# Performance work log

Measured on AMD Instinct MI355X. Metric: run time of the kernel, lower is better.

## Reference

```python
import jax, jax.numpy as jnp
import numpy as np

CHEB = jnp.array([676.5203681218851, -1259.1392167224028, 771.3234287776531,
                  -176.6150291621406, 12.507343278686905, -0.13857109526572012,
                  9.984369578019572e-06, 1.5056327351493116e-07], dtype=jnp.float32)
TWO_PI = float(np.sqrt(2.0 * np.pi))  # sqrt(2*pi), matches torch two_pi constant


def _gamma(z):
    # Lanczos approximation, 8 Chebyshev terms
    x = jnp.full_like(z, 0.9999999999998099)
    for i in range(8):
        x = x + CHEB[i] / (z + (i + 1.0))
    t = z + 8.0 - 0.5
    y = TWO_PI * t ** (z + 0.5) * jnp.exp(-t) * x
    return y / z


def _lower_incl_gamma(s, x, iters=8):
    it = iters - 2
    gs = _gamma(s)
    L = x ** s * gs * jnp.exp(-x)
    gs = gs * s
    R = jnp.reciprocal(gs) * jnp.ones_like(x)
    X = x
    for k in range(it):
        gs = gs * (s + k + 1)
        R = R + X / gs
        X = X * x
    gs = gs * (s + it + 1)
    R = R + X / gs
    return L * R


def _trigamma(x):
    z = x + 1.0
    zz = z * z
    a = 0.2 - jnp.reciprocal(7.0 * zz)
    b = 1.0 - a / zz
    c = 1.0 + b / (3.0 * z)
    d = 1.0 + c / (2.0 * z)
    return d / z + jnp.reciprocal(x * x)


def _k_update(k, s):
    nm = jnp.log(k) - jax.scipy.special.digamma(k) - s
    dn = jnp.reciprocal(k) - _trigamma(k)
    return k - nm / dn


def _compute_ml_est(x, i=10):
    # x: [B, N]; returns per-image k, th of shape [B]
    x = x + 1e-07
    mean_x = jnp.mean(x, axis=1)
    s = jnp.log(mean_x) - jnp.mean(jnp.log(x), axis=1)
    s3 = s - 3.0
    rt = jnp.sqrt(s3 * s3 + 24.0 * s)
    k = (3.0 - s + rt) / (12.0 * s) + 1e-07
    for _ in range(i):
        k = _k_update(k, s)
    k = jnp.clip(k, 1e-07, 18.0)
    th = jnp.reciprocal(k) * mean_x
    return k, th


def setup_inputs() -> dict:
    key = jax.random.key(0)
    x = jax.random.uniform(key, (256, 224, 224), dtype=jnp.float32)
    return {"x": x}


def reference(x):
    B, H, W = x.shape
    xf = x.reshape(B, H * W)
    xf = xf - jnp.min(xf, axis=1, keepdims=True) + 1e-07
    k, th = _compute_ml_est(xf)            # [B], [B]
    kb = k[:, None]                         # broadcast per-image stats over pixels
    y = jnp.reciprocal(_gamma(kb)) * _lower_incl_gamma(kb, xf / th[:, None])
    y = jnp.where(jnp.isfinite(y), y, jnp.zeros_like(y))
    return y.reshape(B, H, W)
```

## Files before the change

kernel.cpp:

```cpp
#include <hip/hip_runtime.h>
#include <math.h>

#define HW   50176
#define NV4  12544
#define TPB  1024

typedef float floatx4 __attribute__((ext_vector_type(4)));

__device__ __forceinline__ float waveMin(float v) {
#pragma unroll
    for (int o = 32; o > 0; o >>= 1) v = fminf(v, __shfl_down(v, o, 64));
    return v;
}
__device__ __forceinline__ double waveSumD(double v) {
#pragma unroll
    for (int o = 32; o > 0; o >>= 1) v += __shfl_down(v, o, 64);
    return v;
}

__device__ __forceinline__ float digamma_f(float x) {
    float r = 0.0f;
#pragma unroll 6
    for (int i = 0; i < 6; ++i) {
        if (x < 6.0f) { r -= __fdividef(1.0f, x); x += 1.0f; }
    }
    float f = __fdividef(1.0f, x * x);
    float ser = f * (1.0f/12.0f - f * (1.0f/120.0f - f * (1.0f/252.0f - f * (1.0f/240.0f - f * (1.0f/132.0f)))));
    return r + logf(x) - 0.5f * __fdividef(1.0f, x) - ser;
}
__device__ __forceinline__ float trigamma_ref(float x) {
    float z = x + 1.0f, zz = z * z;
    float a = 0.2f - __fdividef(1.0f, 7.0f * zz);
    float b = 1.0f - __fdividef(a, zz);
    float c = 1.0f + __fdividef(b, 3.0f * z);
    float d = 1.0f + __fdividef(c, 2.0f * z);
    return __fdividef(d, z) + __fdividef(1.0f, x * x);
}

__global__ void __launch_bounds__(TPB)
gamma_norm2d(const float* __restrict__ x, float* __restrict__ out) {
    const int row = blockIdx.x;
    const int tid = threadIdx.x;
    const float4* __restrict__ xr = (const float4*)(x + (size_t)row * HW);

    const bool extra = (tid < (NV4 - 12 * TPB));

    float4 v[13];
#pragma unroll
    for (int j = 0; j < 12; ++j) v[j] = xr[tid + j * TPB];
    v[12] = extra ? xr[tid + 12 * TPB]
                  : make_float4(INFINITY, INFINITY, INFINITY, INFINITY);

    float pmin = INFINITY, psum = 0.0f;
#pragma unroll
    for (int j = 0; j < 13; ++j) {
        pmin = fminf(pmin, fminf(fminf(v[j].x, v[j].y), fminf(v[j].z, v[j].w)));
        if (j < 12 || extra) psum += (v[j].x + v[j].y) + (v[j].z + v[j].w);
    }
    pmin = waveMin(pmin);
    double dsum = waveSumD((double)psum);

    __shared__ float  smin[16];
    __shared__ double sacc[16];
    __shared__ float  sparams[3];
    __shared__ float  scoef[8];

    const int wid = tid >> 6, lane = tid & 63;
    if (lane == 0) { smin[wid] = pmin; sacc[wid] = dsum; }
    __syncthreads();
    if (tid == 0) {
        float mm = smin[0];
        for (int i = 1; i < 16; ++i) mm = fminf(mm, smin[i]);
        sparams[0] = mm;
    }
    __syncthreads();
    const float rmin = sparams[0];

    float psl = 0.0f;
#pragma unroll
    for (int j = 0; j < 13; ++j) {
        if (j < 12 || extra) {
            psl += (__logf(v[j].x - rmin + 1e-7f + 1e-7f) + __logf(v[j].y - rmin + 1e-7f + 1e-7f))
                 + (__logf(v[j].z - rmin + 1e-7f + 1e-7f) + __logf(v[j].w - rmin + 1e-7f + 1e-7f));
        }
    }
    double dsl = waveSumD((double)psl);
    __shared__ double ssl[16];
    if (lane == 0) ssl[wid] = dsl;
    __syncthreads();

    if (tid == 0) {
        double ts = 0.0, tl = 0.0;
        for (int i = 0; i < 16; ++i) { ts += sacc[i]; tl += ssl[i]; }
        ts -= (double)HW * ((double)rmin - 2e-7);
        const double meand = ts / (double)HW;
        float s = logf((float)meand) - (float)(tl / (double)HW);

        float s3 = s - 3.0f;
        float rt = sqrtf(s3 * s3 + 24.0f * s);
        float k  = __fdividef(3.0f - s + rt, 12.0f * s) + 1e-7f;
#pragma unroll
        for (int it = 0; it < 10; ++it) {
            float nm = logf(k) - digamma_f(k) - s;
            float dn = __fdividef(1.0f, k) - trigamma_ref(k);
            k -= __fdividef(nm, dn);
        }
        if (k < 1e-7f) k = 1e-7f;
        if (k > 18.0f) k = 18.0f;

        const double CH[8] = {676.5203681218851, -1259.1392167224028, 771.3234287776531,
                              -176.6150291621406, 12.507343278686905, -0.13857109526572012,
                              9.984369578019572e-06, 1.5056327351493116e-07};
        double acc = 0.9999999999998099;
#pragma unroll
        for (int i = 0; i < 8; ++i) acc += CH[i] / ((double)k + (double)(i + 1));
        float t  = k + 7.5f;
        float g  = __expf(fmaf(k + 0.5f, __logf(t), -t)) * 2.50662827463f * (float)acc / k;

        float den = g * k;
        scoef[0] = __fdividef(1.0f, den);
#pragma unroll
        for (int j = 1; j < 8; ++j) {
            den *= (k + (float)j);
            scoef[j] = __fdividef(1.0f, den);
        }
        sparams[1] = k;
        sparams[2] = (float)((double)k / meand);
    }
    __syncthreads();

    const float kk = sparams[1], invth = sparams[2];
    const float c0 = scoef[0], c1 = scoef[1], c2 = scoef[2], c3 = scoef[3];
    const float c4 = scoef[4], c5 = scoef[5], c6 = scoef[6], c7 = scoef[7];

    floatx4* __restrict__ yr = (floatx4*)(out + (size_t)row * HW);
#pragma unroll
    for (int j = 0; j < 13; ++j) {
        if (j < 12 || extra) {
            float e[4] = {v[j].x, v[j].y, v[j].z, v[j].w};
            floatx4 o;
#pragma unroll
            for (int q = 0; q < 4; ++q) {
                float xq = (e[q] - rmin + 1e-7f) * invth;
                float p = fmaf(c7, xq, c6);
                p = fmaf(p, xq, c5);
                p = fmaf(p, xq, c4);
                p = fmaf(p, xq, c3);
                p = fmaf(p, xq, c2);
                p = fmaf(p, xq, c1);
                p = fmaf(p, xq, c0);
                float y = __expf(fmaf(kk, __logf(xq), -xq)) * p;
                o[q] = isfinite(y) ? y : 0.0f;
            }
            __builtin_nontemporal_store(o, yr + tid + j * TPB);
        }
    }
}

extern "C" void kernel_launch(void* const* d_in, const int* in_sizes, int n_in,
                              void* d_out, int out_size, void* d_ws, size_t ws_size,
                              hipStream_t stream) {
    const float* x = (const float*)d_in[0];
    float* out = (float*)d_out;
    const int rows = in_sizes[0] / HW;
    gamma_norm2d<<<dim3(rows), dim3(TPB), 0, stream>>>(x, out);
}
```

Before: 110.5 us.

## Split each row across two blocks, re-reading input instead of holding it in registers

Launches two blocks per image row. Each block redundantly computes the full-row min, sum and log-sum statistics, then writes only its half of the output. The row is re-read from global memory (likely L2-resident) in each pass instead of being kept in 52 registers, and launch bounds request 8 waves per SIMD. The aim is more blocks and higher occupancy on a 256-CTU device. The cost is about three times the input reads per row plus duplicated reduction work in both blocks.

```diff
diff --git a/kernel.cpp b/kernel.cpp
--- a/kernel.cpp
+++ b/kernel.cpp
@@ -1,9 +1,11 @@
 #include <hip/hip_runtime.h>
 #include <math.h>
 
-#define HW   50176
-#define NV4  12544
-#define TPB  1024
+#define HW    50176
+#define NV4   12544
+#define HV4   6272
+#define TPB   1024
+#define ROWS  256
 
 typedef float floatx4 __attribute__((ext_vector_type(4)));
 
@@ -37,35 +39,34 @@
     return __fdividef(d, z) + __fdividef(1.0f, x * x);
 }
 
-__global__ void __launch_bounds__(TPB)
+__global__ void __launch_bounds__(TPB, 8)
 gamma_norm2d(const float* __restrict__ x, float* __restrict__ out) {
-    const int row = blockIdx.x;
-    const int tid = threadIdx.x;
+    const int row  = blockIdx.x >> 1;
+    const int half = blockIdx.x & 1;
+    const int tid  = threadIdx.x;
+    const int wid  = tid >> 6, lane = tid & 63;
     const float4* __restrict__ xr = (const float4*)(x + (size_t)row * HW);
 
-    const bool extra = (tid < (NV4 - 12 * TPB));
-
-    float4 v[13];
-#pragma unroll
-    for (int j = 0; j < 12; ++j) v[j] = xr[tid + j * TPB];
-    v[12] = extra ? xr[tid + 12 * TPB]
-                  : make_float4(INFINITY, INFINITY, INFINITY, INFINITY);
+    __shared__ float  smin[16];
+    __shared__ double sacc[16];
+    __shared__ double ssl[16];
+    __shared__ float  sparams[3];
+    __shared__ float  scoef[8];
 
     float pmin = INFINITY, psum = 0.0f;
 #pragma unroll
-    for (int j = 0; j < 13; ++j) {
-        pmin = fminf(pmin, fminf(fminf(v[j].x, v[j].y), fminf(v[j].z, v[j].w)));
-        if (j < 12 || extra) psum += (v[j].x + v[j].y) + (v[j].z + v[j].w);
+    for (int j = 0; j < 12; ++j) {
+        float4 v = xr[j * TPB + tid];
+        pmin = fminf(pmin, fminf(fminf(v.x, v.y), fminf(v.z, v.w)));
+        psum += (v.x + v.y) + (v.z + v.w);
+    }
+    if (tid < 256) {
+        float4 v = xr[12 * TPB + tid];
+        pmin = fminf(pmin, fminf(fminf(v.x, v.y), fminf(v.z, v.w)));
+        psum += (v.x + v.y) + (v.z + v.w);
     }
     pmin = waveMin(pmin);
     double dsum = waveSumD((double)psum);
-
-    __shared__ float  smin[16];
-    __shared__ double sacc[16];
-    __shared__ float  sparams[3];
-    __shared__ float  scoef[8];
-
-    const int wid = tid >> 6, lane = tid & 63;
     if (lane == 0) { smin[wid] = pmin; sacc[wid] = dsum; }
     __syncthreads();
     if (tid == 0) {
@@ -78,14 +79,17 @@
 
     float psl = 0.0f;
 #pragma unroll
-    for (int j = 0; j < 13; ++j) {
-        if (j < 12 || extra) {
-            psl += (__logf(v[j].x - rmin + 1e-7f + 1e-7f) + __logf(v[j].y - rmin + 1e-7f + 1e-7f))
-                 + (__logf(v[j].z - rmin + 1e-7f + 1e-7f) + __logf(v[j].w - rmin + 1e-7f + 1e-7f));
-        }
+    for (int j = 0; j < 12; ++j) {
+        float4 v = xr[j * TPB + tid];
+        psl += (__logf(v.x - rmin + 1e-7f + 1e-7f) + __logf(v.y - rmin + 1e-7f + 1e-7f))
+             + (__logf(v.z - rmin + 1e-7f + 1e-7f) + __logf(v.w - rmin + 1e-7f + 1e-7f));
+    }
+    if (tid < 256) {
+        float4 v = xr[12 * TPB + tid];
+        psl += (__logf(v.x - rmin + 1e-7f + 1e-7f) + __logf(v.y - rmin + 1e-7f + 1e-7f))
+             + (__logf(v.z - rmin + 1e-7f + 1e-7f) + __logf(v.w - rmin + 1e-7f + 1e-7f));
     }
     double dsl = waveSumD((double)psl);
-    __shared__ double ssl[16];
     if (lane == 0) ssl[wid] = dsl;
     __syncthreads();
 
@@ -114,8 +118,8 @@
         double acc = 0.9999999999998099;
 #pragma unroll
         for (int i = 0; i < 8; ++i) acc += CH[i] / ((double)k + (double)(i + 1));
-        float t  = k + 7.5f;
-        float g  = __expf(fmaf(k + 0.5f, __logf(t), -t)) * 2.50662827463f * (float)acc / k;
+        float t = k + 7.5f;
+        float g = __expf(fmaf(k + 0.5f, __logf(t), -t)) * 2.50662827463f * (float)acc / k;
 
         float den = g * k;
         scoef[0] = __fdividef(1.0f, den);
@@ -133,11 +137,14 @@
     const float c0 = scoef[0], c1 = scoef[1], c2 = scoef[2], c3 = scoef[3];
     const float c4 = scoef[4], c5 = scoef[5], c6 = scoef[6], c7 = scoef[7];
 
-    floatx4* __restrict__ yr = (floatx4*)(out + (size_t)row * HW);
+    const float4* __restrict__ xh = xr + (size_t)half * HV4;
+    floatx4* __restrict__ yh = (floatx4*)(out + (size_t)row * HW) + (size_t)half * HV4;
+
 #pragma unroll
-    for (int j = 0; j < 13; ++j) {
-        if (j < 12 || extra) {
-            float e[4] = {v[j].x, v[j].y, v[j].z, v[j].w};
+    for (int j = 0; j < 7; ++j) {
+        if (j < 6 || tid < 128) {
+            float4 v = xh[j * TPB + tid];
+            float e[4] = {v.x, v.y, v.z, v.w};
             floatx4 o;
 #pragma unroll
             for (int q = 0; q < 4; ++q) {
@@ -152,7 +159,7 @@
                 float y = __expf(fmaf(kk, __logf(xq), -xq)) * p;
                 o[q] = isfinite(y) ? y : 0.0f;
             }
-            __builtin_nontemporal_store(o, yr + tid + j * TPB);
+            __builtin_nontemporal_store(o, yh + j * TPB + tid);
         }
     }
 }
@@ -163,5 +170,5 @@
     const float* x = (const float*)d_in[0];
     float* out = (float*)d_out;
     const int rows = in_sizes[0] / HW;
-    gamma_norm2d<<<dim3(rows), dim3(TPB), 0, stream>>>(x, out);
+    gamma_norm2d<<<dim3(rows * 2), dim3(TPB), 0, stream>>>(x, out);
 }
```

After: 127.9 us. 1.16x slower.
